# Kernel tuning notes

Hardware: AMD Instinct MI355X
Metric: run time of the kernel (lower is better)

The kernel has to match this reference:

```python
import jax, jax.numpy as jnp
import numpy as np
from jax import lax

EPS = 1e-5

def conv2d(x, w, groups=1, pad=0):
    return lax.conv_general_dilated(
        x, w, window_strides=(1, 1), padding=[(pad, pad), (pad, pad)],
        dimension_numbers=('NCHW', 'OIHW', 'NCHW'), feature_group_count=groups)

def setup_inputs() -> dict:
    key = jax.random.key(0)
    ks = jax.random.split(key, 10)
    B, C, H, W = 8, 64, 128, 128
    s = 0.05
    f32 = jnp.float32
    return {
        'x': jax.random.normal(ks[0], (B, C, H, W), f32),
        # key_embed: Conv2d(64,64,3,groups=8,bias=False) -> weight [64, 64/8, 3, 3]
        'w_key': jax.random.normal(ks[1], (64, 8, 3, 3), f32) * s,
        # embed[0]: Conv2d(128,32,1,groups=2,bias=False) -> [32, 128/2, 1, 1]
        'w_e1': jax.random.normal(ks[2], (32, 64, 1, 1), f32) * s,
        # embed[2]: Conv2d(32,72,1,groups=2,bias=True) -> [72, 32/2, 1, 1]
        'w_e2': jax.random.normal(ks[3], (72, 16, 1, 1), f32) * s,
        'b_e2': jax.random.normal(ks[4], (72,), f32) * s,
        # GroupNorm(num_groups=8, num_channels=72) affine params
        'gn_w': jnp.ones((72,), f32),
        'gn_b': jnp.zeros((72,), f32),
        # conv1x1: Conv2d(64,64,1,groups=2,bias=False) -> [64, 32, 1, 1]
        'w_c1': jax.random.normal(ks[5], (64, 32, 1, 1), f32) * s,
        # conv_du: Conv2d(64,4,1,bias=False), Conv2d(4,64,1,bias=False)
        'w_du1': jax.random.normal(ks[6], (4, 64, 1, 1), f32) * s,
        'w_du2': jax.random.normal(ks[7], (64, 4, 1, 1), f32) * s,
    }

def reference(x, w_key, w_e1, w_e2, b_e2, gn_w, gn_b, w_c1, w_du1, w_du2):
    B, C, H, W = x.shape  # C == 64
    KK = 9                # kernel_size^2
    # key embedding: grouped 3x3 conv + ReLU
    k = jax.nn.relu(conv2d(x, w_key, groups=8, pad=1))
    # interleave x and k along channels: view of [B,64,2,H,W] -> [B,128,H,W]
    qk = jnp.stack([x, k], axis=2).reshape(B, 2 * C, H, W)
    # dynamic kernel generation (embed)
    w = jax.nn.relu(conv2d(qk, w_e1, groups=2))
    w = conv2d(w, w_e2, groups=2) + b_e2[None, :, None, None]  # [B,72,H,W]
    # GroupNorm(8, 72): normalize over (channels-in-group, H, W)
    wg = w.reshape(B, 8, 9, H, W)
    m = wg.mean(axis=(2, 3, 4), keepdims=True)
    v = wg.var(axis=(2, 3, 4), keepdims=True)
    w = ((wg - m) * lax.rsqrt(v + EPS)).reshape(B, 72, H, W)
    w = w * gn_w[None, :, None, None] + gn_b[None, :, None, None]
    # per-pixel kernels: [B*2, 4, 9, H, W]
    w = w.reshape(B * 2, 4, KK, H, W)
    # value path
    xv = conv2d(x, w_c1, groups=2).reshape(B * 2, 32, H, W)
    # unfold 3x3 patches with zero padding 1 -> [B*2, 32, 9, H, W]
    xp = jnp.pad(xv, ((0, 0), (0, 0), (1, 1), (1, 1)))
    patches = jnp.stack(
        [xp[:, :, i:i + H, j:j + W] for i in range(3) for j in range(3)], axis=2)
    # share_planes=8: 8 channels share each kernel -> [B*2, 4, 8, 9, H, W]
    patches = patches.reshape(B * 2, 4, 8, KK, H, W)
    out = jnp.einsum('bgckhw,bgkhw->bgchw', patches, w)  # local conv
    out = out.reshape(B, C, H, W)
    # channel attention
    y = out.mean(axis=(2, 3))                 # [B, 64]
    y = jax.nn.relu(y @ w_du1[:, :, 0, 0].T)  # [B, 4]
    y = jax.nn.sigmoid(y @ w_du2[:, :, 0, 0].T)  # [B, 64]
    return out * y[:, :, None, None]
```

## Files before the change

kernel.cpp:

```cpp
#include <hip/hip_runtime.h>
#include <math.h>

#define Hd 128
#define Wd 128
#define HW 16384

__device__ __forceinline__ float wred(float v) {
  #pragma unroll
  for (int o = 32; o > 0; o >>= 1) v += __shfl_down(v, o, 64);
  return v;
}

__global__ __launch_bounds__(256) void k_keyconv(const float* __restrict__ x,
                                                 const float* __restrict__ wkey,
                                                 float* __restrict__ kout) {
  __shared__ float xt[8][34][24];
  const int tid = threadIdx.x;
  const int tx = tid & 15, ty = tid >> 4;
  const int b = blockIdx.z >> 3, g = blockIdx.z & 7;
  const int h0 = blockIdx.y * 32, w0 = blockIdx.x * 16;
  for (int i = tid; i < 8 * 612; i += 256) {
    int ch = i / 612, r = i - ch * 612;
    int yy = r / 18, xx = r - yy * 18;
    int gh = h0 + yy - 1, gw = w0 + xx - 1;
    float v = 0.f;
    if (gh >= 0 && gh < Hd && gw >= 0 && gw < Wd)
      v = x[((long)(b * 64 + g * 8 + ch) << 14) + (gh << 7) + gw];
    xt[ch][yy][xx] = v;
  }
  __syncthreads();
  float acc0[8] = {0.f, 0.f, 0.f, 0.f, 0.f, 0.f, 0.f, 0.f};
  float acc1[8] = {0.f, 0.f, 0.f, 0.f, 0.f, 0.f, 0.f, 0.f};
  const float* wg = wkey + g * 576;
  #pragma unroll
  for (int ich = 0; ich < 8; ++ich) {
    float nb[12];
    #pragma unroll
    for (int rr = 0; rr < 4; ++rr)
      #pragma unroll
      for (int cc = 0; cc < 3; ++cc)
        nb[rr * 3 + cc] = xt[ich][2 * ty + rr][tx + cc];
    #pragma unroll
    for (int oc = 0; oc < 8; ++oc) {
      const float* wr = wg + oc * 72 + ich * 9;
      #pragma unroll
      for (int dy = 0; dy < 3; ++dy)
        #pragma unroll
        for (int dx = 0; dx < 3; ++dx) {
          float wv = wr[dy * 3 + dx];
          acc0[oc] += wv * nb[dy * 3 + dx];
          acc1[oc] += wv * nb[(dy + 1) * 3 + dx];
        }
    }
  }
  const int h = h0 + 2 * ty, w = w0 + tx;
  #pragma unroll
  for (int oc = 0; oc < 8; ++oc) {
    const long base = ((long)(b * 64 + g * 8 + oc) << 14);
    kout[base + (h << 7) + w] = fmaxf(acc0[oc], 0.f);
    kout[base + ((h + 1) << 7) + w] = fmaxf(acc1[oc], 0.f);
  }
}

__global__ __launch_bounds__(128) void k_embed(const float* __restrict__ x,
                                               float* __restrict__ kxv,
                                               const float* __restrict__ we1,
                                               const float* __restrict__ we2,
                                               const float* __restrict__ be2,
                                               const float* __restrict__ wc1,
                                               float* __restrict__ wpre,
                                               float* __restrict__ spart) {
  const int tid = threadIdx.x;
  const int p = blockIdx.x * 128 + tid;
  const int b = blockIdx.y;
  const int s = blockIdx.z;
  float xc[32], kc[32];
  #pragma unroll
  for (int j = 0; j < 32; ++j) {
    xc[j] = x[((long)(b * 64 + 32 * s + j) << 14) + p];
    kc[j] = kxv[((long)(b * 64 + 32 * s + j) << 14) + p];
  }
  #pragma unroll 4
  for (int o = 0; o < 32; ++o) {
    const float* wr = wc1 + (32 * s + o) * 32;
    float a = 0.f;
    #pragma unroll
    for (int j = 0; j < 32; ++j) a += wr[j] * xc[j];
    kxv[((long)(b * 64 + 32 * s + o) << 14) + p] = a;
  }
  float w1a[16];
  #pragma unroll
  for (int o = 0; o < 16; ++o) {
    const float* wr = we1 + (16 * s + o) * 64;
    float a = 0.f;
    #pragma unroll
    for (int j = 0; j < 32; ++j) a += wr[2 * j] * xc[j] + wr[2 * j + 1] * kc[j];
    w1a[o] = fmaxf(a, 0.f);
  }
  const int row = blockIdx.x * 2 + (tid >> 6);
  #pragma unroll
  for (int gl = 0; gl < 4; ++gl) {
    float lgs = 0.f, lgq = 0.f;
    #pragma unroll
    for (int kk = 0; kk < 9; ++kk) {
      const int oc2 = 36 * s + gl * 9 + kk;
      const float* wr = we2 + oc2 * 16;
      float a = be2[oc2];
      #pragma unroll
      for (int ic = 0; ic < 16; ++ic) a += wr[ic] * w1a[ic];
      wpre[((long)(b * 72 + oc2) << 14) + p] = a;
      lgs += a;
      lgq += a * a;
    }
    float r1 = wred(lgs), r2 = wred(lgq);
    if ((tid & 63) == 0) {
      spart[row * 128 + (b * 8 + 4 * s + gl) * 2 + 0] = r1;
      spart[row * 128 + (b * 8 + 4 * s + gl) * 2 + 1] = r2;
    }
  }
}

__global__ void k_gnstat(const float* __restrict__ spart, float* __restrict__ minv) {
  __shared__ float sred[128];
  const int t = threadIdx.x;
  float a = 0.f;
  #pragma unroll 8
  for (int r = 0; r < 256; ++r) a += spart[r * 128 + t];
  sred[t] = a;
  __syncthreads();
  if (t < 64) {
    const float N = 9.f * (float)HW;
    float s = sred[2 * t], q = sred[2 * t + 1];
    float m = s / N;
    float var = q / N - m * m;
    minv[2 * t] = m;
    minv[2 * t + 1] = rsqrtf(var + 1e-5f);
  }
}

__global__ __launch_bounds__(256) void k_local(const float* __restrict__ kxv,
                                               const float* __restrict__ wpre,
                                               const float* __restrict__ minv,
                                               const float* __restrict__ gnw,
                                               const float* __restrict__ gnb,
                                               float* __restrict__ out,
                                               float* __restrict__ part) {
  __shared__ float xt[8][34][24];
  const int tid = threadIdx.x;
  const int tx = tid & 15, ty = tid >> 4;
  const int z = blockIdx.z;
  const int b2 = z >> 2, g = z & 3;
  const int t = b2 & 1, b = b2 >> 1;
  const int h0 = blockIdx.y * 32, w0 = blockIdx.x * 16;
  for (int i = tid; i < 8 * 612; i += 256) {
    int ch = i / 612, r = i - ch * 612;
    int yy = r / 18, xx = r - yy * 18;
    int gh = h0 + yy - 1, gw = w0 + xx - 1;
    float v = 0.f;
    if (gh >= 0 && gh < Hd && gw >= 0 && gw < Wd)
      v = kxv[((long)(b2 * 32 + g * 8 + ch) << 14) + (gh << 7) + gw];
    xt[ch][yy][xx] = v;
  }
  __syncthreads();
  const int gg = 4 * t + g;
  const float m = minv[(b * 8 + gg) * 2];
  const float inv = minv[(b * 8 + gg) * 2 + 1];
  const int p0 = ((h0 + 2 * ty) << 7) + (w0 + tx);
  const int p1 = p0 + 128;
  float wn0[9], wn1[9];
  #pragma unroll
  for (int kk = 0; kk < 9; ++kk) {
    const int ch72 = 36 * t + 9 * g + kk;
    const long base = ((long)(b * 72 + ch72) << 14);
    const float sc = inv * gnw[ch72], sh = gnb[ch72] - m * inv * gnw[ch72];
    wn0[kk] = wpre[base + p0] * sc + sh;
    wn1[kk] = wpre[base + p1] * sc + sh;
  }
  const int prow = (blockIdx.y * 8 + blockIdx.x) * 4 + (tid >> 6);
  #pragma unroll
  for (int cc = 0; cc < 8; ++cc) {
    float nb[12];
    #pragma unroll
    for (int rr = 0; rr < 4; ++rr)
      #pragma unroll
      for (int ccol = 0; ccol < 3; ++ccol)
        nb[rr * 3 + ccol] = xt[cc][2 * ty + rr][tx + ccol];
    float o0 = 0.f, o1 = 0.f;
    #pragma unroll
    for (int dy = 0; dy < 3; ++dy)
      #pragma unroll
      for (int dx = 0; dx < 3; ++dx) {
        o0 += wn0[dy * 3 + dx] * nb[dy * 3 + dx];
        o1 += wn1[dy * 3 + dx] * nb[(dy + 1) * 3 + dx];
      }
    const int ch512 = b2 * 32 + g * 8 + cc;
    out[((long)ch512 << 14) + p0] = o0;
    out[((long)ch512 << 14) + p1] = o1;
    float os = wred(o0 + o1);
    if ((tid & 63) == 0) part[prow * 512 + ch512] = os;
  }
}

__global__ void k_ca(const float* __restrict__ part, const float* __restrict__ du1,
                     const float* __restrict__ du2, float* __restrict__ ys) {
  __shared__ float sy[8][64];
  __shared__ float sy4[8][4];
  const int tid = threadIdx.x;
  const int b = tid >> 6, c = tid & 63;
  float acc = 0.f;
  #pragma unroll 8
  for (int r = 0; r < 128; ++r) acc += part[r * 512 + tid];
  sy[b][c] = acc * (1.f / (float)HW);
  __syncthreads();
  if (tid < 32) {
    int bb = tid >> 2, j = tid & 3;
    float a = 0.f;
    for (int c2 = 0; c2 < 64; ++c2) a += sy[bb][c2] * du1[j * 64 + c2];
    sy4[bb][j] = fmaxf(a, 0.f);
  }
  __syncthreads();
  float z = 0.f;
  #pragma unroll
  for (int j = 0; j < 4; ++j) z += sy4[b][j] * du2[c * 4 + j];
  ys[tid] = 1.f / (1.f + expf(-z));
}

__global__ __launch_bounds__(256) void k_scale(float* __restrict__ out,
                                               const float* __restrict__ ys) {
  const long i4 = (long)blockIdx.x * 256 + threadIdx.x;
  const long e = i4 * 4;
  const int bc = (int)(e >> 14);
  const float s = ys[bc];
  float4* o = (float4*)out;
  float4 v = o[i4];
  v.x *= s; v.y *= s; v.z *= s; v.w *= s;
  o[i4] = v;
}

extern "C" void kernel_launch(void* const* d_in, const int* in_sizes, int n_in,
                              void* d_out, int out_size, void* d_ws, size_t ws_size,
                              hipStream_t stream) {
  const float* x    = (const float*)d_in[0];
  const float* wkey = (const float*)d_in[1];
  const float* we1  = (const float*)d_in[2];
  const float* we2  = (const float*)d_in[3];
  const float* be2  = (const float*)d_in[4];
  const float* gnw  = (const float*)d_in[5];
  const float* gnb  = (const float*)d_in[6];
  const float* wc1  = (const float*)d_in[7];
  const float* du1  = (const float*)d_in[8];
  const float* du2  = (const float*)d_in[9];
  float* out = (float*)d_out;
  float* ws = (float*)d_ws;

  float* kxv  = ws;
  float* wpre = ws + 8388608;
  float* part = ws + 17825792;
  float* spart = part;
  float* minv = part + 131072;
  float* ys   = minv + 128;

  k_keyconv<<<dim3(8, 4, 64), 256, 0, stream>>>(x, wkey, kxv);
  k_embed<<<dim3(128, 8, 2), 128, 0, stream>>>(x, kxv, we1, we2, be2, wc1, wpre, spart);
  k_gnstat<<<1, 128, 0, stream>>>(spart, minv);
  k_local<<<dim3(8, 4, 64), 256, 0, stream>>>(kxv, wpre, minv, gnw, gnb, out, part);
  k_ca<<<1, 512, 0, stream>>>(part, du1, du2, ys);
  k_scale<<<8192, 256, 0, stream>>>(out, ys);
}
```

Baseline: 241.1 us.

## Fuse key conv into embed kernel to avoid key tensor round trip

The grouped 3x3 key convolution is merged into the embed kernel. Each block now computes the key activations for a 16x16 tile in registers, looping over four channel groups with a shared-memory halo tile, instead of writing k to global memory and reading it back. The GroupNorm partial sums are also reduced across waves in shared memory before being written, which shrinks the partial-sum array that k_gnstat reads. In exchange the 3x3 conv has less register reuse, since each thread now produces one output row instead of two, and halo loads are repeated per group while register pressure rises.

```diff
diff --git a/kernel.cpp b/kernel.cpp
--- a/kernel.cpp
+++ b/kernel.cpp
@@ -11,74 +11,56 @@
   return v;
 }
 
-__global__ __launch_bounds__(256) void k_keyconv(const float* __restrict__ x,
-                                                 const float* __restrict__ wkey,
-                                                 float* __restrict__ kout) {
-  __shared__ float xt[8][34][24];
+__global__ __launch_bounds__(256, 4) void k_fused(const float* __restrict__ x,
+                                                  const float* __restrict__ wkey,
+                                                  const float* __restrict__ we1,
+                                                  const float* __restrict__ we2,
+                                                  const float* __restrict__ be2,
+                                                  const float* __restrict__ wc1,
+                                                  float* __restrict__ xv,
+                                                  float* __restrict__ wpre,
+                                                  float* __restrict__ spart) {
+  __shared__ float xt[8][18][24];
+  __shared__ float sred2[4][8];
   const int tid = threadIdx.x;
   const int tx = tid & 15, ty = tid >> 4;
-  const int b = blockIdx.z >> 3, g = blockIdx.z & 7;
-  const int h0 = blockIdx.y * 32, w0 = blockIdx.x * 16;
-  for (int i = tid; i < 8 * 612; i += 256) {
-    int ch = i / 612, r = i - ch * 612;
-    int yy = r / 18, xx = r - yy * 18;
-    int gh = h0 + yy - 1, gw = w0 + xx - 1;
-    float v = 0.f;
-    if (gh >= 0 && gh < Hd && gw >= 0 && gw < Wd)
-      v = x[((long)(b * 64 + g * 8 + ch) << 14) + (gh << 7) + gw];
-    xt[ch][yy][xx] = v;
-  }
-  __syncthreads();
-  float acc0[8] = {0.f, 0.f, 0.f, 0.f, 0.f, 0.f, 0.f, 0.f};
-  float acc1[8] = {0.f, 0.f, 0.f, 0.f, 0.f, 0.f, 0.f, 0.f};
-  const float* wg = wkey + g * 576;
-  #pragma unroll
-  for (int ich = 0; ich < 8; ++ich) {
-    float nb[12];
-    #pragma unroll
-    for (int rr = 0; rr < 4; ++rr)
-      #pragma unroll
-      for (int cc = 0; cc < 3; ++cc)
-        nb[rr * 3 + cc] = xt[ich][2 * ty + rr][tx + cc];
-    #pragma unroll
-    for (int oc = 0; oc < 8; ++oc) {
-      const float* wr = wg + oc * 72 + ich * 9;
-      #pragma unroll
-      for (int dy = 0; dy < 3; ++dy)
+  const int b = blockIdx.y, s = blockIdx.z;
+  const int h0 = (blockIdx.x >> 3) * 16, w0 = (blockIdx.x & 7) * 16;
+  const int p = ((h0 + ty) << 7) + (w0 + tx);
+  float xc[32], kc[32];
+  #pragma unroll
+  for (int g = 0; g < 4; ++g) {
+    for (int i = tid; i < 8 * 324; i += 256) {
+      int ch = i / 324, r = i - ch * 324;
+      int yy = r / 18, xx = r - yy * 18;
+      int gh = h0 + yy - 1, gw = w0 + xx - 1;
+      float v = 0.f;
+      if (gh >= 0 && gh < Hd && gw >= 0 && gw < Wd)
+        v = x[((long)(b * 64 + 32 * s + 8 * g + ch) << 14) + (gh << 7) + gw];
+      xt[ch][yy][xx] = v;
+    }
+    __syncthreads();
+    float kacc[8] = {0.f, 0.f, 0.f, 0.f, 0.f, 0.f, 0.f, 0.f};
+    const float* wg = wkey + (4 * s + g) * 576;
+    #pragma unroll
+    for (int ich = 0; ich < 8; ++ich) {
+      float nb[9];
+      #pragma unroll
+      for (int rr = 0; rr < 3; ++rr)
         #pragma unroll
-        for (int dx = 0; dx < 3; ++dx) {
-          float wv = wr[dy * 3 + dx];
-          acc0[oc] += wv * nb[dy * 3 + dx];
-          acc1[oc] += wv * nb[(dy + 1) * 3 + dx];
-        }
-    }
-  }
-  const int h = h0 + 2 * ty, w = w0 + tx;
-  #pragma unroll
-  for (int oc = 0; oc < 8; ++oc) {
-    const long base = ((long)(b * 64 + g * 8 + oc) << 14);
-    kout[base + (h << 7) + w] = fmaxf(acc0[oc], 0.f);
-    kout[base + ((h + 1) << 7) + w] = fmaxf(acc1[oc], 0.f);
-  }
-}
-
-__global__ __launch_bounds__(128) void k_embed(const float* __restrict__ x,
-                                               float* __restrict__ kxv,
-                                               const float* __restrict__ we1,
-                                               const float* __restrict__ we2,
-                                               const float* __restrict__ be2,
-                                               const float* __restrict__ wc1,
-                                               float* __restrict__ wpre,
-                                               float* __restrict__ spart) {
-  const int tid = threadIdx.x;
-  const int p = blockIdx.x * 128 + tid;
-  const int b = blockIdx.y;
-  const int s = blockIdx.z;
-  float xc[32], kc[32];
-  #pragma unroll
-  for (int j = 0; j < 32; ++j) {
-    xc[j] = x[((long)(b * 64 + 32 * s + j) << 14) + p];
-    kc[j] = kxv[((long)(b * 64 + 32 * s + j) << 14) + p];
+        for (int cc = 0; cc < 3; ++cc)
+          nb[rr * 3 + cc] = xt[ich][ty + rr][tx + cc];
+      xc[8 * g + ich] = nb[4];
+      #pragma unroll
+      for (int oc = 0; oc < 8; ++oc) {
+        const float* wr = wg + oc * 72 + ich * 9;
+        #pragma unroll
+        for (int k9 = 0; k9 < 9; ++k9) kacc[oc] += wr[k9] * nb[k9];
+      }
+    }
+    #pragma unroll
+    for (int oc = 0; oc < 8; ++oc) kc[8 * g + oc] = fmaxf(kacc[oc], 0.f);
+    __syncthreads();
   }
   #pragma unroll 4
   for (int o = 0; o < 32; ++o) {
@@ -86,7 +68,7 @@
     float a = 0.f;
     #pragma unroll
     for (int j = 0; j < 32; ++j) a += wr[j] * xc[j];
-    kxv[((long)(b * 64 + 32 * s + o) << 14) + p] = a;
+    xv[((long)(b * 64 + 32 * s + o) << 14) + p] = a;
   }
   float w1a[16];
   #pragma unroll
@@ -97,7 +79,6 @@
     for (int j = 0; j < 32; ++j) a += wr[2 * j] * xc[j] + wr[2 * j + 1] * kc[j];
     w1a[o] = fmaxf(a, 0.f);
   }
-  const int row = blockIdx.x * 2 + (tid >> 6);
   #pragma unroll
   for (int gl = 0; gl < 4; ++gl) {
     float lgs = 0.f, lgq = 0.f;
@@ -114,9 +95,14 @@
     }
     float r1 = wred(lgs), r2 = wred(lgq);
     if ((tid & 63) == 0) {
-      spart[row * 128 + (b * 8 + 4 * s + gl) * 2 + 0] = r1;
-      spart[row * 128 + (b * 8 + 4 * s + gl) * 2 + 1] = r2;
-    }
+      sred2[tid >> 6][2 * gl] = r1;
+      sred2[tid >> 6][2 * gl + 1] = r2;
+    }
+  }
+  __syncthreads();
+  if (tid < 8) {
+    float a = sred2[0][tid] + sred2[1][tid] + sred2[2][tid] + sred2[3][tid];
+    spart[blockIdx.x * 128 + b * 16 + s * 8 + tid] = a;
   }
 }
 
@@ -125,7 +111,7 @@
   const int t = threadIdx.x;
   float a = 0.f;
   #pragma unroll 8
-  for (int r = 0; r < 256; ++r) a += spart[r * 128 + t];
+  for (int r = 0; r < 64; ++r) a += spart[r * 128 + t];
   sred[t] = a;
   __syncthreads();
   if (t < 64) {
@@ -260,8 +246,7 @@
   float* minv = part + 131072;
   float* ys   = minv + 128;
 
-  k_keyconv<<<dim3(8, 4, 64), 256, 0, stream>>>(x, wkey, kxv);
-  k_embed<<<dim3(128, 8, 2), 128, 0, stream>>>(x, kxv, we1, we2, be2, wc1, wpre, spart);
+  k_fused<<<dim3(64, 8, 2), 256, 0, stream>>>(x, wkey, we1, we2, be2, wc1, kxv, wpre, spart);
   k_gnstat<<<1, 128, 0, stream>>>(spart, minv);
   k_local<<<dim3(8, 4, 64), 256, 0, stream>>>(kxv, wpre, minv, gnw, gnb, out, part);
   k_ca<<<1, 512, 0, stream>>>(part, du1, du2, ys);
```

New measurement: 233.3 us. 3.2% less time.
